# Optimization experiments

Hardware: AMD Instinct MI355X
Metric: run time of the kernel (lower is better)

## Reference

```python
import jax, jax.numpy as jnp
import numpy as np

DT = 0.02
Z_DIM = 32
U_DIM = 16


def _mlp(x, layers):
    # layers: list of (W, b); SiLU between all but last layer
    n = len(layers)
    for i, (W, b) in enumerate(layers):
        x = x @ W + b
        if i < n - 1:
            x = jax.nn.silu(x)
    return x


def _forward(x, u,
             e_w1, e_b1, e_w2, e_b2, e_w3, e_b3,
             d_w1, d_b1, d_w2, d_b2, d_w3, d_b3, d_w4, d_b4,
             a_w1, a_b1, a_w2, a_b2, a_w3, a_b3,
             b_w1, b_b1, b_w2, b_b2, b_w3, b_b3):
    # encode
    z = _mlp(x, [(e_w1, e_b1), (e_w2, e_b2), (e_w3, e_b3)])          # (B, Z)
    # state-dependent A(x) parameters: pairs (a_i, b_i) per 2x2 block
    aux = _mlp(x, [(a_w1, a_b1), (a_w2, a_b2), (a_w3, a_b3)])        # (B, Z)
    a = aux[:, 0::2]                                                  # (B, Z/2)
    b = aux[:, 1::2]
    f = jnp.exp(a * DT)
    c = jnp.cos(b * DT)
    s = jnp.sin(b * DT)
    # A(x) @ z without materializing block-diagonal: per-pair rotation-scale
    z0 = z[:, 0::2]
    z1 = z[:, 1::2]
    Az = jnp.stack([f * (c * z0 - s * z1), f * (s * z0 + c * z1)], axis=-1).reshape(z.shape)
    # B(x) @ u
    Bmat = _mlp(x, [(b_w1, b_b1), (b_w2, b_b2), (b_w3, b_b3)]).reshape(-1, Z_DIM, U_DIM)
    Bu = jnp.einsum('bzu,bu->bz', Bmat, u)
    # latent Euler step + decode
    z_next = z + DT * (Az + Bu)
    return _mlp(z_next, [(d_w1, d_b1), (d_w2, d_b2), (d_w3, d_b3), (d_w4, d_b4)])


def setup_inputs() -> dict:
    key = jax.random.key(0)
    ks = iter(jax.random.split(key, 32))
    def w(shape, scale=0.02):
        return jax.random.normal(next(ks), shape, jnp.float32) * scale
    B, X, U, Z, H, A = 16384, 64, 16, 32, 1024, 256
    return {
        'x': jax.random.normal(next(ks), (B, X), jnp.float32),
        'u': jax.random.normal(next(ks), (B, U), jnp.float32),
        'e_w1': w((X, H)), 'e_b1': w((H,)),
        'e_w2': w((H, H)), 'e_b2': w((H,)),
        'e_w3': w((H, Z)), 'e_b3': w((Z,)),
        'd_w1': w((Z, H)), 'd_b1': w((H,)),
        'd_w2': w((H, H)), 'd_b2': w((H,)),
        'd_w3': w((H, H)), 'd_b3': w((H,)),
        'd_w4': w((H, X)), 'd_b4': w((X,)),
        'a_w1': w((X, A)), 'a_b1': w((A,)),
        'a_w2': w((A, A)), 'a_b2': w((A,)),
        'a_w3': w((A, Z)), 'a_b3': w((Z,)),
        'b_w1': w((X, A)), 'b_b1': w((A,)),
        'b_w2': w((A, A)), 'b_b2': w((A,)),
        'b_w3': w((A, Z * U)), 'b_b3': w((Z * U,)),
    }


def reference(x, u,
              e_w1, e_b1, e_w2, e_b2, e_w3, e_b3,
              d_w1, d_b1, d_w2, d_b2, d_w3, d_b3, d_w4, d_b4,
              a_w1, a_b1, a_w2, a_b2, a_w3, a_b3,
              b_w1, b_b1, b_w2, b_b2, b_w3, b_b3):
    return _forward(x, u,
                    e_w1, e_b1, e_w2, e_b2, e_w3, e_b3,
                    d_w1, d_b1, d_w2, d_b2, d_w3, d_b3, d_w4, d_b4,
                    a_w1, a_b1, a_w2, a_b2, a_w3, a_b3,
                    b_w1, b_b1, b_w2, b_b2, b_w3, b_b3)
```

## Files before the change

kernel.cpp:

```cpp
#include <hip/hip_runtime.h>
#include <cstdint>
#include <cstddef>

#define B_SZ 16384
#define X_D  64
#define U_D  16
#define Z_D  32
#define H_D  1024
#define A_D  256
#define DT_C 0.02f

typedef _Float16 f16;
typedef f16   f16x8 __attribute__((ext_vector_type(8)));
typedef f16   f16x4 __attribute__((ext_vector_type(4)));
typedef float f32x4 __attribute__((ext_vector_type(4)));

#define AS1 __attribute__((address_space(1)))
#define AS3 __attribute__((address_space(3)))

__device__ __forceinline__ void gld_lds16(const void* g, void* l) {
    __builtin_amdgcn_global_load_lds((AS1 void*)(g), (AS3 void*)(l), 16, 0, 0);
}

struct GArg {
    const f16*  A;
    const f16*  W;
    const float* bias;
    void*       C;
    const float* U;
    int lda, ldc, K;
};
struct GPair { GArg g[2]; };

template<int BM,int BN,int BK,int WM,int WN,bool SILU,int OM>
__launch_bounds__(256)
__global__ void gemm_k(GPair p)
{
    static_assert(OM != 1 || BN == 128, "OM1 repack assumes BN=128");
    const GArg ga = p.g[blockIdx.z];

    constexpr int SEGROW = BK / 8;
    constexpr int SMASK  = (SEGROW < 8 ? SEGROW : 8) - 1;
    constexpr int WTM = BM / WM, WTN = BN / WN;
    constexpr int RM = WTM / 16, RN = WTN / 16;
    constexpr int ITA = (BM * SEGROW) / 256;
    constexpr int ITB = (BN * SEGROW) / 256;

    constexpr int STAGE_B = (BM + BN) * BK * 2;
    constexpr int CS_B    = (OM == 1) ? BM * BN * 2 : 0;
    constexpr int SMEM_B  = STAGE_B > CS_B ? STAGE_B : CS_B;
    __shared__ __align__(16) char smem[SMEM_B];
    f16* As = (f16*)smem;
    f16* Bs = As + BM * BK;

    const int tid  = threadIdx.x;
    const int lane = tid & 63;
    const int wave = tid >> 6;
    const int wm = wave / WN, wn = wave % WN;
    const int l15 = lane & 15, quad = lane >> 4;

    const size_t arow0 = (size_t)blockIdx.x * BM;
    const size_t brow0 = (size_t)blockIdx.y * BN;
    const int lda = ga.lda, K = ga.K;

    f32x4 zero = {0.f, 0.f, 0.f, 0.f};
    f32x4 acc[RM][RN];
#pragma unroll
    for (int i = 0; i < RM; ++i)
#pragma unroll
        for (int j = 0; j < RN; ++j) acc[i][j] = zero;

    for (int k0 = 0; k0 < K; k0 += BK) {
#pragma unroll
        for (int it = 0; it < ITA; ++it) {
            int s = it * 256 + tid;
            int row = s / SEGROW, st = s % SEGROW;
            int sg = st ^ (row & SMASK);
            gld_lds16(ga.A + (arow0 + row) * lda + k0 + sg * 8, &As[s * 8]);
        }
#pragma unroll
        for (int it = 0; it < ITB; ++it) {
            int s = it * 256 + tid;
            int row = s / SEGROW, st = s % SEGROW;
            int sg = st ^ (row & SMASK);
            gld_lds16(ga.W + (brow0 + row) * K + k0 + sg * 8, &Bs[s * 8]);
        }
        __syncthreads();

#pragma unroll
        for (int kk = 0; kk < BK; kk += 32) {
            f16x8 af[RM], bf[RN];
#pragma unroll
            for (int i = 0; i < RM; ++i) {
                int row = wm * WTM + i * 16 + l15;
                int st  = ((kk >> 3) + quad) ^ (row & SMASK);
                af[i] = *(const f16x8*)&As[(row * SEGROW + st) * 8];
            }
#pragma unroll
            for (int j = 0; j < RN; ++j) {
                int row = wn * WTN + j * 16 + l15;
                int st  = ((kk >> 3) + quad) ^ (row & SMASK);
                bf[j] = *(const f16x8*)&Bs[(row * SEGROW + st) * 8];
            }
#pragma unroll
            for (int i = 0; i < RM; ++i)
#pragma unroll
                for (int j = 0; j < RN; ++j)
                    acc[i][j] = __builtin_amdgcn_mfma_f32_16x16x32_f16(
                        af[i], bf[j], acc[i][j], 0, 0, 0);
        }
        __syncthreads();
    }

    const int rowbL = wm * WTM;
    const int colbL = wn * WTN;

    if constexpr (OM == 2) {
        const int zcol0 = ((int)brow0 + colbL) >> 4;
#pragma unroll
        for (int i = 0; i < RM; ++i) {
#pragma unroll
            for (int r = 0; r < 4; ++r) {
                int row = (int)arow0 + rowbL + i * 16 + quad * 4 + r;
                float uv = ga.U[row * 16 + l15];
#pragma unroll
                for (int j = 0; j < RN; ++j) {
                    int col = (int)brow0 + colbL + j * 16 + l15;
                    float v = (acc[i][j][r] + ga.bias[col]) * uv;
                    v += __shfl_xor(v, 8, 16);
                    v += __shfl_xor(v, 4, 16);
                    v += __shfl_xor(v, 2, 16);
                    v += __shfl_xor(v, 1, 16);
                    if (l15 == 0) ((float*)ga.C)[row * 32 + zcol0 + j] = v;
                }
            }
        }
    } else if constexpr (OM == 1) {
        f16* Cs = (f16*)smem;
#pragma unroll
        for (int j = 0; j < RN; ++j) {
            int colL = colbL + j * 16 + l15;
            float bv = ga.bias[(int)brow0 + colL];
            int chL = colL >> 3, wi = colL & 7;
#pragma unroll
            for (int i = 0; i < RM; ++i) {
#pragma unroll
                for (int r = 0; r < 4; ++r) {
                    int rowL = rowbL + i * 16 + quad * 4 + r;
                    float v = acc[i][j][r] + bv;
                    if (SILU) v = v / (1.0f + __expf(-v));
                    Cs[rowL * BN + ((chL ^ (rowL & 15)) << 3) + wi] = (f16)v;
                }
            }
        }
        __syncthreads();
        f16* Cout = (f16*)ga.C;
#pragma unroll
        for (int pass = 0; pass < (BM * BN / 8) / 256; ++pass) {
            int s = pass * 256 + tid;
            int rowL = s >> 4;
            int ch = s & 15;
            f16x8 v = *(const f16x8*)&Cs[rowL * BN + ((ch ^ (rowL & 15)) << 3)];
            *(f16x8*)&Cout[(size_t)(arow0 + rowL) * ga.ldc + brow0 + ch * 8] = v;
        }
    } else {
        float* Cout = (float*)ga.C;
#pragma unroll
        for (int j = 0; j < RN; ++j) {
            int col = (int)brow0 + colbL + j * 16 + l15;
            float bv = ga.bias[col];
#pragma unroll
            for (int i = 0; i < RM; ++i) {
#pragma unroll
                for (int r = 0; r < 4; ++r) {
                    int row = (int)arow0 + rowbL + i * 16 + quad * 4 + r;
                    float v = acc[i][j][r] + bv;
                    if (SILU) v = v / (1.0f + __expf(-v));
                    Cout[(size_t)row * ga.ldc + col] = v;
                }
            }
        }
    }
}

struct PrepArgs {
    const float* w[13];
    f16*         wt[13];
    int          K[13];
    int          N[13];
    const float* bsrc[3];
    float*       bias1;
    const float* x;
    f16*         xb;
};

__launch_bounds__(256)
__global__ void prep_k(PrepArgs pa, int ntrans, int ncvt)
{
    int bid = blockIdx.x;
    if (bid < ntrans) {
        int i = 0, t;
        for (;; ++i) {
            t = (pa.K[i] >> 5) * (pa.N[i] >> 5);
            if (bid < t) break;
            bid -= t;
        }
        const int K = pa.K[i], N = pa.N[i];
        const int tn = N >> 5;
        const int k0 = (bid / tn) << 5, n0 = (bid % tn) << 5;
        __shared__ float tbuf[32][33];
        const int tx = threadIdx.x & 31, ty = threadIdx.x >> 5;
        const float* src = pa.w[i];
        f16* dst = pa.wt[i];
#pragma unroll
        for (int r = 0; r < 32; r += 8)
            tbuf[ty + r][tx] = src[(size_t)(k0 + ty + r) * N + n0 + tx];
        __syncthreads();
#pragma unroll
        for (int r = 0; r < 32; r += 8)
            dst[(size_t)(n0 + ty + r) * K + k0 + tx] = (f16)tbuf[tx][ty + r];
    } else if (bid < ntrans + ncvt) {
        int i = ((bid - ntrans) * 256 + threadIdx.x) * 4;
        float4 v = *(const float4*)(pa.x + i);
        f16x4 o = {(f16)v.x, (f16)v.y, (f16)v.z, (f16)v.w};
        *(f16x4*)(pa.xb + i) = o;
    } else {
        int idx = (bid - ntrans - ncvt) * 256 + (int)threadIdx.x;
        float v = (idx < 1024) ? pa.bsrc[0][idx]
                : (idx < 1280) ? pa.bsrc[1][idx - 1024]
                               : pa.bsrc[2][idx - 1280];
        pa.bias1[idx] = v;
    }
}

__global__ void koopman_k(const float* __restrict__ zf, const float* __restrict__ auxf,
                          const float* __restrict__ Buf, f16* __restrict__ zn)
{
    int idx = blockIdx.x * 256 + threadIdx.x;
    int zi = idx & 31;
    int base = idx & ~1;
    float a = auxf[base], b = auxf[base + 1];
    float f = __expf(a * DT_C);
    float c = __cosf(b * DT_C);
    float s = __sinf(b * DT_C);
    float z0 = zf[base], z1 = zf[base + 1];
    float Az = (zi & 1) ? f * (s * z0 + c * z1) : f * (c * z0 - s * z1);
    zn[idx] = (f16)(zf[idx] + DT_C * (Az + Buf[idx]));
}

extern "C" void kernel_launch(void* const* d_in, const int* in_sizes, int n_in,
                              void* d_out, int out_size, void* d_ws, size_t ws_size,
                              hipStream_t stream)
{
    (void)in_sizes; (void)n_in; (void)out_size; (void)ws_size;
    const float* x    = (const float*)d_in[0];
    const float* u    = (const float*)d_in[1];
    const float* e_w1 = (const float*)d_in[2];  const float* e_b1 = (const float*)d_in[3];
    const float* e_w2 = (const float*)d_in[4];  const float* e_b2 = (const float*)d_in[5];
    const float* e_w3 = (const float*)d_in[6];  const float* e_b3 = (const float*)d_in[7];
    const float* d_w1 = (const float*)d_in[8];  const float* d_b1 = (const float*)d_in[9];
    const float* d_w2 = (const float*)d_in[10]; const float* d_b2 = (const float*)d_in[11];
    const float* d_w3 = (const float*)d_in[12]; const float* d_b3 = (const float*)d_in[13];
    const float* d_w4 = (const float*)d_in[14]; const float* d_b4 = (const float*)d_in[15];
    const float* a_w1 = (const float*)d_in[16]; const float* a_b1 = (const float*)d_in[17];
    const float* a_w2 = (const float*)d_in[18]; const float* a_b2 = (const float*)d_in[19];
    const float* a_w3 = (const float*)d_in[20]; const float* a_b3 = (const float*)d_in[21];
    const float* b_w1 = (const float*)d_in[22]; const float* b_b1 = (const float*)d_in[23];
    const float* b_w2 = (const float*)d_in[24]; const float* b_b2 = (const float*)d_in[25];
    const float* b_w3 = (const float*)d_in[26]; const float* b_b3 = (const float*)d_in[27];

    char* p = (char*)d_ws;
    auto alloc = [&](size_t nbytes) -> void* {
        void* r = (void*)p;
        p += (nbytes + 255) & ~(size_t)255;
        return r;
    };
    f16*   xb   = (f16*)  alloc((size_t)B_SZ * X_D * 2);
    f16*   cc1  = (f16*)  alloc((size_t)B_SZ * 1536 * 2);
    f16*   cc2  = (f16*)  alloc((size_t)B_SZ * 1536 * 2);
    float* zf   = (float*)alloc((size_t)B_SZ * Z_D * 4);
    float* auxf = (float*)alloc((size_t)B_SZ * Z_D * 4);
    float* Buf  = (float*)alloc((size_t)B_SZ * Z_D * 4);
    f16*   znb  = (f16*)  alloc((size_t)B_SZ * Z_D * 2);
    f16*   h1d  = cc1;
    f16*   h2d  = cc2;
    f16*   h3d  = cc1;
    f16*   W1t   = (f16*)alloc((size_t)1536 * X_D * 2);
    float* bias1 = (float*)alloc(1536 * 4);
    f16* e_w2t = (f16*)alloc((size_t)H_D * H_D * 2);
    f16* e_w3t = (f16*)alloc((size_t)Z_D * H_D * 2);
    f16* d_w1t = (f16*)alloc((size_t)H_D * Z_D * 2);
    f16* d_w2t = (f16*)alloc((size_t)H_D * H_D * 2);
    f16* d_w3t = (f16*)alloc((size_t)H_D * H_D * 2);
    f16* d_w4t = (f16*)alloc((size_t)X_D * H_D * 2);
    f16* a_w2t = (f16*)alloc((size_t)A_D * A_D * 2);
    f16* a_w3t = (f16*)alloc((size_t)Z_D * A_D * 2);
    f16* b_w2t = (f16*)alloc((size_t)A_D * A_D * 2);
    f16* b_w3t = (f16*)alloc((size_t)(Z_D * U_D) * A_D * 2);

    PrepArgs pa;
    const float* ws_[13] = {e_w1, e_w2, e_w3, d_w1, d_w2, d_w3, d_w4,
                            a_w1, a_w2, a_w3, b_w1, b_w2, b_w3};
    f16* wts_[13] = {W1t, e_w2t, e_w3t, d_w1t, d_w2t, d_w3t, d_w4t,
                     W1t + (size_t)1024 * X_D, a_w2t, a_w3t,
                     W1t + (size_t)1280 * X_D, b_w2t, b_w3t};
    int Ks_[13] = {X_D, H_D, H_D, Z_D, H_D, H_D, H_D, X_D, A_D, A_D, X_D, A_D, A_D};
    int Ns_[13] = {H_D, H_D, Z_D, H_D, H_D, H_D, X_D, A_D, A_D, Z_D, A_D, A_D, Z_D*U_D};
    int ntrans = 0;
    for (int i = 0; i < 13; ++i) {
        pa.w[i] = ws_[i]; pa.wt[i] = wts_[i]; pa.K[i] = Ks_[i]; pa.N[i] = Ns_[i];
        ntrans += (Ks_[i] >> 5) * (Ns_[i] >> 5);
    }
    pa.bsrc[0] = e_b1; pa.bsrc[1] = a_b1; pa.bsrc[2] = b_b1;
    pa.bias1 = bias1; pa.x = x; pa.xb = xb;
    const int ncvt = (B_SZ * X_D) / 1024;
    prep_k<<<ntrans + ncvt + 6, 256, 0, stream>>>(pa, ntrans, ncvt);

    auto G = [](const f16* A, const f16* W, const float* bias, void* C,
                int lda, int ldc, int K, const float* U = nullptr) {
        GArg g; g.A = A; g.W = W; g.bias = bias; g.C = C; g.U = U;
        g.lda = lda; g.ldc = ldc; g.K = K; return g;
    };
    GPair pr;

    pr.g[0] = pr.g[1] = G(xb, W1t, bias1, cc1, X_D, 1536, X_D);
    gemm_k<128,128,64,2,2,true,1><<<dim3(B_SZ/128, 1536/128, 1), 256, 0, stream>>>(pr);

    pr.g[0] = pr.g[1] = G(cc1, e_w2t, e_b2, cc2, 1536, 1536, H_D);
    gemm_k<128,128,64,2,2,true,1><<<dim3(B_SZ/128, H_D/128, 1), 256, 0, stream>>>(pr);

    pr.g[0] = G(cc1 + 1024, a_w2t, a_b2, cc2 + 1024, 1536, 1536, A_D);
    pr.g[1] = G(cc1 + 1280, b_w2t, b_b2, cc2 + 1280, 1536, 1536, A_D);
    gemm_k<128,128,64,2,2,true,1><<<dim3(B_SZ/128, A_D/128, 2), 256, 0, stream>>>(pr);

    pr.g[0] = G(cc2,        e_w3t, e_b3, zf,   1536, Z_D, H_D);
    pr.g[1] = G(cc2 + 1024, a_w3t, a_b3, auxf, 1536, Z_D, A_D);
    gemm_k<64,32,64,4,1,false,0><<<dim3(B_SZ/64, 1, 2), 256, 0, stream>>>(pr);

    pr.g[0] = pr.g[1] = G(cc2 + 1280, b_w3t, b_b3, Buf, 1536, Z_D, A_D, u);
    gemm_k<128,128,64,2,2,false,2><<<dim3(B_SZ/128, (Z_D*U_D)/128, 1), 256, 0, stream>>>(pr);

    koopman_k<<<(B_SZ * Z_D) / 256, 256, 0, stream>>>(zf, auxf, Buf, znb);

    pr.g[0] = pr.g[1] = G(znb, d_w1t, d_b1, h1d, Z_D, H_D, Z_D);
    gemm_k<128,128,32,2,2,true,1><<<dim3(B_SZ/128, H_D/128, 1), 256, 0, stream>>>(pr);

    pr.g[0] = pr.g[1] = G(h1d, d_w2t, d_b2, h2d, H_D, H_D, H_D);
    gemm_k<128,128,64,2,2,true,1><<<dim3(B_SZ/128, H_D/128, 1), 256, 0, stream>>>(pr);

    pr.g[0] = pr.g[1] = G(h2d, d_w3t, d_b3, h3d, H_D, H_D, H_D);
    gemm_k<128,128,64,2,2,true,1><<<dim3(B_SZ/128, H_D/128, 1), 256, 0, stream>>>(pr);

    pr.g[0] = pr.g[1] = G(h3d, d_w4t, d_b4, d_out, H_D, X_D, H_D);
    gemm_k<64,64,64,2,2,false,0><<<dim3(B_SZ/64, 1, 1), 256, 0, stream>>>(pr);
}
```

Before: 378.6 us.

## Use 256-row GEMM tiles and fuse Koopman step into Bu GEMM epilogue

Doubles the M tile of all main GEMMs from 128 to 256 rows. Each wave now holds twice as many accumulators, and the LDS-staged epilogue writes out in two 128-row passes to keep shared memory small. Separately, the latent Euler/rotation update is folded into the B(x)u GEMM epilogue, so the standalone koopman kernel and the Buf intermediate buffer are gone. This saves launches and global traffic and improves operand reuse, at the cost of more register pressure, possibly lower occupancy, and fewer blocks per grid.

```diff
diff --git a/kernel.cpp b/kernel.cpp
--- a/kernel.cpp
+++ b/kernel.cpp
@@ -28,6 +28,8 @@
     const float* bias;
     void*       C;
     const float* U;
+    const float* zf;
+    const float* aux;
     int lda, ldc, K;
 };
 struct GPair { GArg g[2]; };
@@ -36,7 +38,7 @@
 __launch_bounds__(256)
 __global__ void gemm_k(GPair p)
 {
-    static_assert(OM != 1 || BN == 128, "OM1 repack assumes BN=128");
+    static_assert(OM != 1 || (BM == 256 && BN == 128 && WM == 2), "OM1 shape");
     const GArg ga = p.g[blockIdx.z];
 
     constexpr int SEGROW = BK / 8;
@@ -47,7 +49,7 @@
     constexpr int ITB = (BN * SEGROW) / 256;
 
     constexpr int STAGE_B = (BM + BN) * BK * 2;
-    constexpr int CS_B    = (OM == 1) ? BM * BN * 2 : 0;
+    constexpr int CS_B    = (OM == 1) ? 128 * BN * 2 : 0;
     constexpr int SMEM_B  = STAGE_B > CS_B ? STAGE_B : CS_B;
     __shared__ __align__(16) char smem[SMEM_B];
     f16* As = (f16*)smem;
@@ -131,37 +133,55 @@
                     v += __shfl_xor(v, 4, 16);
                     v += __shfl_xor(v, 2, 16);
                     v += __shfl_xor(v, 1, 16);
-                    if (l15 == 0) ((float*)ga.C)[row * 32 + zcol0 + j] = v;
+                    if (l15 == 0) {
+                        int z = zcol0 + j;
+                        int pb = row * 32 + (z & ~1);
+                        float a  = ga.aux[pb], b = ga.aux[pb + 1];
+                        float z0 = ga.zf[pb],  z1 = ga.zf[pb + 1];
+                        float f  = __expf(a * DT_C);
+                        float c_ = __cosf(b * DT_C);
+                        float s_ = __sinf(b * DT_C);
+                        float Az = (z & 1) ? f * (s_ * z0 + c_ * z1)
+                                           : f * (c_ * z0 - s_ * z1);
+                        float zc = (z & 1) ? z1 : z0;
+                        ((f16*)ga.C)[row * 32 + z] = (f16)(zc + DT_C * (Az + v));
+                    }
                 }
             }
         }
     } else if constexpr (OM == 1) {
         f16* Cs = (f16*)smem;
-#pragma unroll
-        for (int j = 0; j < RN; ++j) {
-            int colL = colbL + j * 16 + l15;
-            float bv = ga.bias[(int)brow0 + colL];
-            int chL = colL >> 3, wi = colL & 7;
-#pragma unroll
-            for (int i = 0; i < RM; ++i) {
-#pragma unroll
-                for (int r = 0; r < 4; ++r) {
-                    int rowL = rowbL + i * 16 + quad * 4 + r;
-                    float v = acc[i][j][r] + bv;
-                    if (SILU) v = v / (1.0f + __expf(-v));
-                    Cs[rowL * BN + ((chL ^ (rowL & 15)) << 3) + wi] = (f16)v;
+        f16* Cout = (f16*)ga.C;
+#pragma unroll
+        for (int pass = 0; pass < 2; ++pass) {
+            if (wm == pass) {
+#pragma unroll
+                for (int j = 0; j < RN; ++j) {
+                    int colL = wn * WTN + j * 16 + l15;
+                    float bv = ga.bias[(int)brow0 + colL];
+                    int chL = colL >> 3, wi = colL & 7;
+#pragma unroll
+                    for (int i = 0; i < RM; ++i) {
+#pragma unroll
+                        for (int r = 0; r < 4; ++r) {
+                            int rowL = i * 16 + quad * 4 + r;
+                            float v = acc[i][j][r] + bv;
+                            if (SILU) v = v / (1.0f + __expf(-v));
+                            Cs[rowL * BN + ((chL ^ (rowL & 15)) << 3) + wi] = (f16)v;
+                        }
+                    }
                 }
             }
-        }
-        __syncthreads();
-        f16* Cout = (f16*)ga.C;
-#pragma unroll
-        for (int pass = 0; pass < (BM * BN / 8) / 256; ++pass) {
-            int s = pass * 256 + tid;
-            int rowL = s >> 4;
-            int ch = s & 15;
-            f16x8 v = *(const f16x8*)&Cs[rowL * BN + ((ch ^ (rowL & 15)) << 3)];
-            *(f16x8*)&Cout[(size_t)(arow0 + rowL) * ga.ldc + brow0 + ch * 8] = v;
+            __syncthreads();
+#pragma unroll
+            for (int it = 0; it < (128 * BN / 8) / 256; ++it) {
+                int s = it * 256 + tid;
+                int rowL = s >> 4, ch = s & 15;
+                f16x8 v = *(const f16x8*)&Cs[rowL * BN + ((ch ^ (rowL & 15)) << 3)];
+                *(f16x8*)&Cout[(size_t)(arow0 + pass * 128 + rowL) * ga.ldc
+                               + brow0 + ch * 8] = v;
+            }
+            __syncthreads();
         }
     } else {
         float* Cout = (float*)ga.C;
@@ -231,21 +251,6 @@
                                : pa.bsrc[2][idx - 1280];
         pa.bias1[idx] = v;
     }
-}
-
-__global__ void koopman_k(const float* __restrict__ zf, const float* __restrict__ auxf,
-                          const float* __restrict__ Buf, f16* __restrict__ zn)
-{
-    int idx = blockIdx.x * 256 + threadIdx.x;
-    int zi = idx & 31;
-    int base = idx & ~1;
-    float a = auxf[base], b = auxf[base + 1];
-    float f = __expf(a * DT_C);
-    float c = __cosf(b * DT_C);
-    float s = __sinf(b * DT_C);
-    float z0 = zf[base], z1 = zf[base + 1];
-    float Az = (zi & 1) ? f * (s * z0 + c * z1) : f * (c * z0 - s * z1);
-    zn[idx] = (f16)(zf[idx] + DT_C * (Az + Buf[idx]));
 }
 
 extern "C" void kernel_launch(void* const* d_in, const int* in_sizes, int n_in,
@@ -280,7 +285,6 @@
     f16*   cc2  = (f16*)  alloc((size_t)B_SZ * 1536 * 2);
     float* zf   = (float*)alloc((size_t)B_SZ * Z_D * 4);
     float* auxf = (float*)alloc((size_t)B_SZ * Z_D * 4);
-    float* Buf  = (float*)alloc((size_t)B_SZ * Z_D * 4);
     f16*   znb  = (f16*)  alloc((size_t)B_SZ * Z_D * 2);
     f16*   h1d  = cc1;
     f16*   h2d  = cc2;
@@ -317,39 +321,38 @@
     prep_k<<<ntrans + ncvt + 6, 256, 0, stream>>>(pa, ntrans, ncvt);
 
     auto G = [](const f16* A, const f16* W, const float* bias, void* C,
-                int lda, int ldc, int K, const float* U = nullptr) {
+                int lda, int ldc, int K, const float* U = nullptr,
+                const float* zf_ = nullptr, const float* aux_ = nullptr) {
         GArg g; g.A = A; g.W = W; g.bias = bias; g.C = C; g.U = U;
-        g.lda = lda; g.ldc = ldc; g.K = K; return g;
+        g.zf = zf_; g.aux = aux_; g.lda = lda; g.ldc = ldc; g.K = K; return g;
     };
     GPair pr;
 
     pr.g[0] = pr.g[1] = G(xb, W1t, bias1, cc1, X_D, 1536, X_D);
-    gemm_k<128,128,64,2,2,true,1><<<dim3(B_SZ/128, 1536/128, 1), 256, 0, stream>>>(pr);
+    gemm_k<256,128,64,2,2,true,1><<<dim3(B_SZ/256, 1536/128, 1), 256, 0, stream>>>(pr);
 
     pr.g[0] = pr.g[1] = G(cc1, e_w2t, e_b2, cc2, 1536, 1536, H_D);
-    gemm_k<128,128,64,2,2,true,1><<<dim3(B_SZ/128, H_D/128, 1), 256, 0, stream>>>(pr);
+    gemm_k<256,128,64,2,2,true,1><<<dim3(B_SZ/256, H_D/128, 1), 256, 0, stream>>>(pr);
 
     pr.g[0] = G(cc1 + 1024, a_w2t, a_b2, cc2 + 1024, 1536, 1536, A_D);
     pr.g[1] = G(cc1 + 1280, b_w2t, b_b2, cc2 + 1280, 1536, 1536, A_D);
-    gemm_k<128,128,64,2,2,true,1><<<dim3(B_SZ/128, A_D/128, 2), 256, 0, stream>>>(pr);
+    gemm_k<256,128,64,2,2,true,1><<<dim3(B_SZ/256, A_D/128, 2), 256, 0, stream>>>(pr);
 
     pr.g[0] = G(cc2,        e_w3t, e_b3, zf,   1536, Z_D, H_D);
     pr.g[1] = G(cc2 + 1024, a_w3t, a_b3, auxf, 1536, Z_D, A_D);
     gemm_k<64,32,64,4,1,false,0><<<dim3(B_SZ/64, 1, 2), 256, 0, stream>>>(pr);
 
-    pr.g[0] = pr.g[1] = G(cc2 + 1280, b_w3t, b_b3, Buf, 1536, Z_D, A_D, u);
-    gemm_k<128,128,64,2,2,false,2><<<dim3(B_SZ/128, (Z_D*U_D)/128, 1), 256, 0, stream>>>(pr);
-
-    koopman_k<<<(B_SZ * Z_D) / 256, 256, 0, stream>>>(zf, auxf, Buf, znb);
+    pr.g[0] = pr.g[1] = G(cc2 + 1280, b_w3t, b_b3, znb, 1536, Z_D, A_D, u, zf, auxf);
+    gemm_k<256,128,64,2,2,false,2><<<dim3(B_SZ/256, (Z_D*U_D)/128, 1), 256, 0, stream>>>(pr);
 
     pr.g[0] = pr.g[1] = G(znb, d_w1t, d_b1, h1d, Z_D, H_D, Z_D);
-    gemm_k<128,128,32,2,2,true,1><<<dim3(B_SZ/128, H_D/128, 1), 256, 0, stream>>>(pr);
+    gemm_k<256,128,32,2,2,true,1><<<dim3(B_SZ/256, H_D/128, 1), 256, 0, stream>>>(pr);
 
     pr.g[0] = pr.g[1] = G(h1d, d_w2t, d_b2, h2d, H_D, H_D, H_D);
-    gemm_k<128,128,64,2,2,true,1><<<dim3(B_SZ/128, H_D/128, 1), 256, 0, stream>>>(pr);
+    gemm_k<256,128,64,2,2,true,1><<<dim3(B_SZ/256, H_D/128, 1), 256, 0, stream>>>(pr);
 
     pr.g[0] = pr.g[1] = G(h2d, d_w3t, d_b3, h3d, H_D, H_D, H_D);
-    gemm_k<128,128,64,2,2,true,1><<<dim3(B_SZ/128, H_D/128, 1), 256, 0, stream>>>(pr);
+    gemm_k<256,128,64,2,2,true,1><<<dim3(B_SZ/256, H_D/128, 1), 256, 0, stream>>>(pr);
 
     pr.g[0] = pr.g[1] = G(h3d, d_w4t, d_b4, d_out, H_D, X_D, H_D);
     gemm_k<64,64,64,2,2,false,0><<<dim3(B_SZ/64, 1, 1), 256, 0, stream>>>(pr);
```

New measurement: 674.4 us. 1.78x slower.

## Fuse latent heads and Koopman step into one kernel; merge layer-2 GEMMs

Applied to the files above, without the earlier changes.

Replaces the encoder output GEMM, aux output GEMM, B(x)u GEMM and the Koopman elementwise kernel with a single mid_k kernel that works on 32-row tiles and keeps z, aux and Bu in shared memory before writing the f16 latent. It also merges the three second-layer GEMMs (encoder, aux, B-net) into one launch using a y-index split across three argument sets. This cuts kernel launches and the fp32 intermediate round-trips through global memory. The cost is a small-tile fused kernel with lower MFMA efficiency, in which the B-head weights are reloaded per 32-row block.

```diff
diff --git a/kernel.cpp b/kernel.cpp
--- a/kernel.cpp
+++ b/kernel.cpp
@@ -27,17 +27,18 @@
     const f16*  W;
     const float* bias;
     void*       C;
-    const float* U;
     int lda, ldc, K;
 };
-struct GPair { GArg g[2]; };
+struct GSet { GArg g[3]; int yn0, yn1; };
 
 template<int BM,int BN,int BK,int WM,int WN,bool SILU,int OM>
 __launch_bounds__(256)
-__global__ void gemm_k(GPair p)
+__global__ void gemm_k(GSet p)
 {
     static_assert(OM != 1 || BN == 128, "OM1 repack assumes BN=128");
-    const GArg ga = p.g[blockIdx.z];
+    int yb = blockIdx.y, gi = 0;
+    if (yb >= p.yn0) { yb -= p.yn0; gi = 1; if (yb >= p.yn1) { yb -= p.yn1; gi = 2; } }
+    const GArg ga = p.g[gi];
 
     constexpr int SEGROW = BK / 8;
     constexpr int SMASK  = (SEGROW < 8 ? SEGROW : 8) - 1;
@@ -60,7 +61,7 @@
     const int l15 = lane & 15, quad = lane >> 4;
 
     const size_t arow0 = (size_t)blockIdx.x * BM;
-    const size_t brow0 = (size_t)blockIdx.y * BN;
+    const size_t brow0 = (size_t)yb * BN;
     const int lda = ga.lda, K = ga.K;
 
     f32x4 zero = {0.f, 0.f, 0.f, 0.f};
@@ -115,27 +116,7 @@
     const int rowbL = wm * WTM;
     const int colbL = wn * WTN;
 
-    if constexpr (OM == 2) {
-        const int zcol0 = ((int)brow0 + colbL) >> 4;
-#pragma unroll
-        for (int i = 0; i < RM; ++i) {
-#pragma unroll
-            for (int r = 0; r < 4; ++r) {
-                int row = (int)arow0 + rowbL + i * 16 + quad * 4 + r;
-                float uv = ga.U[row * 16 + l15];
-#pragma unroll
-                for (int j = 0; j < RN; ++j) {
-                    int col = (int)brow0 + colbL + j * 16 + l15;
-                    float v = (acc[i][j][r] + ga.bias[col]) * uv;
-                    v += __shfl_xor(v, 8, 16);
-                    v += __shfl_xor(v, 4, 16);
-                    v += __shfl_xor(v, 2, 16);
-                    v += __shfl_xor(v, 1, 16);
-                    if (l15 == 0) ((float*)ga.C)[row * 32 + zcol0 + j] = v;
-                }
-            }
-        }
-    } else if constexpr (OM == 1) {
+    if constexpr (OM == 1) {
         f16* Cs = (f16*)smem;
 #pragma unroll
         for (int j = 0; j < RN; ++j) {
@@ -180,6 +161,149 @@
                 }
             }
         }
+    }
+}
+
+__launch_bounds__(256)
+__global__ void mid_k(const f16* __restrict__ cc2,
+                      const f16* __restrict__ e_w3t, const float* __restrict__ e_b3,
+                      const f16* __restrict__ a_w3t, const float* __restrict__ a_b3,
+                      const f16* __restrict__ b_w3t, const float* __restrict__ b_b3,
+                      const float* __restrict__ u,   f16* __restrict__ znb)
+{
+    __shared__ __align__(16) f16 As[32 * 64];
+    __shared__ __align__(16) f16 Bs[128 * 64];
+    __shared__ float zb[32 * 32];
+    __shared__ float ab[32 * 32];
+    __shared__ float bu[32 * 32];
+    __shared__ float ub[32 * 16];
+
+    const int tid  = threadIdx.x;
+    const int lane = tid & 63, wave = tid >> 6;
+    const int l15 = lane & 15, quad = lane >> 4;
+    const int r0 = blockIdx.x * 32;
+
+    ub[tid]       = u[r0 * 16 + tid];
+    ub[tid + 256] = u[r0 * 16 + 256 + tid];
+
+#pragma unroll 1
+    for (int ph = 0; ph < 2; ++ph) {
+        const f16* W    = ph ? a_w3t : e_w3t;
+        const float* bs = ph ? a_b3 : e_b3;
+        const int K     = ph ? 256 : 1024;
+        const int co    = ph ? 1024 : 0;
+        float* ob       = ph ? ab : zb;
+        f32x4 acc = {0.f, 0.f, 0.f, 0.f};
+        for (int k0 = 0; k0 < K; k0 += 64) {
+            {
+                int row = tid >> 3, sg = (tid & 7) ^ (row & 7);
+                gld_lds16(cc2 + (size_t)(r0 + row) * 1536 + co + k0 + sg * 8,
+                          &As[tid * 8]);
+            }
+            {
+                int row = tid >> 3, sg = (tid & 7) ^ (row & 7);
+                gld_lds16(W + (size_t)row * K + k0 + sg * 8, &Bs[tid * 8]);
+            }
+            __syncthreads();
+#pragma unroll
+            for (int kk = 0; kk < 64; kk += 32) {
+                int ar = ((wave >> 1) << 4) + l15;
+                int ast = ((kk >> 3) + quad) ^ (ar & 7);
+                f16x8 af = *(const f16x8*)&As[(ar * 8 + ast) * 8];
+                int br = ((wave & 1) << 4) + l15;
+                int bst = ((kk >> 3) + quad) ^ (br & 7);
+                f16x8 bf = *(const f16x8*)&Bs[(br * 8 + bst) * 8];
+                acc = __builtin_amdgcn_mfma_f32_16x16x32_f16(af, bf, acc, 0, 0, 0);
+            }
+            __syncthreads();
+        }
+#pragma unroll
+        for (int r = 0; r < 4; ++r) {
+            int row = ((wave >> 1) << 4) + quad * 4 + r;
+            int col = ((wave & 1) << 4) + l15;
+            ob[row * 32 + col] = acc[r] + bs[col];
+        }
+    }
+
+#pragma unroll 1
+    for (int ch = 0; ch < 4; ++ch) {
+        f32x4 acc[2][2];
+#pragma unroll
+        for (int i = 0; i < 2; ++i)
+#pragma unroll
+            for (int j = 0; j < 2; ++j) acc[i][j] = f32x4{0.f, 0.f, 0.f, 0.f};
+        for (int k0 = 0; k0 < 256; k0 += 64) {
+            {   int row = tid >> 3, sg = (tid & 7) ^ (row & 7);
+                gld_lds16(cc2 + (size_t)(r0 + row) * 1536 + 1280 + k0 + sg * 8,
+                          &As[tid * 8]);
+            }
+#pragma unroll
+            for (int it = 0; it < 4; ++it) {
+                int s = it * 256 + tid;
+                int row = s >> 3, sg = (s & 7) ^ (row & 7);
+                gld_lds16(b_w3t + (size_t)(ch * 128 + row) * 256 + k0 + sg * 8,
+                          &Bs[s * 8]);
+            }
+            __syncthreads();
+#pragma unroll
+            for (int kk = 0; kk < 64; kk += 32) {
+                f16x8 af[2], bf[2];
+#pragma unroll
+                for (int i = 0; i < 2; ++i) {
+                    int ar = i * 16 + l15;
+                    int st = ((kk >> 3) + quad) ^ (ar & 7);
+                    af[i] = *(const f16x8*)&As[(ar * 8 + st) * 8];
+                }
+#pragma unroll
+                for (int j = 0; j < 2; ++j) {
+                    int br = wave * 32 + j * 16 + l15;
+                    int st = ((kk >> 3) + quad) ^ (br & 7);
+                    bf[j] = *(const f16x8*)&Bs[(br * 8 + st) * 8];
+                }
+#pragma unroll
+                for (int i = 0; i < 2; ++i)
+#pragma unroll
+                    for (int j = 0; j < 2; ++j)
+                        acc[i][j] = __builtin_amdgcn_mfma_f32_16x16x32_f16(
+                            af[i], bf[j], acc[i][j], 0, 0, 0);
+            }
+            __syncthreads();
+        }
+#pragma unroll
+        for (int j = 0; j < 2; ++j) {
+            int colg = ch * 128 + wave * 32 + j * 16 + l15;
+            float bv = b_b3[colg];
+            int z = colg >> 4;
+#pragma unroll
+            for (int i = 0; i < 2; ++i) {
+#pragma unroll
+                for (int r = 0; r < 4; ++r) {
+                    int row = i * 16 + quad * 4 + r;
+                    float v = (acc[i][j][r] + bv) * ub[row * 16 + l15];
+                    v += __shfl_xor(v, 8, 16);
+                    v += __shfl_xor(v, 4, 16);
+                    v += __shfl_xor(v, 2, 16);
+                    v += __shfl_xor(v, 1, 16);
+                    if (l15 == 0) bu[row * 32 + z] = v;
+                }
+            }
+        }
+    }
+    __syncthreads();
+
+#pragma unroll
+    for (int t = 0; t < 4; ++t) {
+        int idx = t * 256 + tid;
+        int row = idx >> 5, z = idx & 31;
+        int pb = idx & ~1;
+        float a  = ab[pb], b = ab[pb + 1];
+        float z0 = zb[pb], z1 = zb[pb + 1];
+        float f  = __expf(a * DT_C);
+        float c_ = __cosf(b * DT_C);
+        float s_ = __sinf(b * DT_C);
+        float Az = (z & 1) ? f * (s_ * z0 + c_ * z1) : f * (c_ * z0 - s_ * z1);
+        float zc = (z & 1) ? z1 : z0;
+        znb[(size_t)(r0 + row) * 32 + z] = (f16)(zc + DT_C * (Az + bu[idx]));
     }
 }
 
@@ -231,21 +355,6 @@
                                : pa.bsrc[2][idx - 1280];
         pa.bias1[idx] = v;
     }
-}
-
-__global__ void koopman_k(const float* __restrict__ zf, const float* __restrict__ auxf,
-                          const float* __restrict__ Buf, f16* __restrict__ zn)
-{
-    int idx = blockIdx.x * 256 + threadIdx.x;
-    int zi = idx & 31;
-    int base = idx & ~1;
-    float a = auxf[base], b = auxf[base + 1];
-    float f = __expf(a * DT_C);
-    float c = __cosf(b * DT_C);
-    float s = __sinf(b * DT_C);
-    float z0 = zf[base], z1 = zf[base + 1];
-    float Az = (zi & 1) ? f * (s * z0 + c * z1) : f * (c * z0 - s * z1);
-    zn[idx] = (f16)(zf[idx] + DT_C * (Az + Buf[idx]));
 }
 
 extern "C" void kernel_launch(void* const* d_in, const int* in_sizes, int n_in,
@@ -278,9 +387,6 @@
     f16*   xb   = (f16*)  alloc((size_t)B_SZ * X_D * 2);
     f16*   cc1  = (f16*)  alloc((size_t)B_SZ * 1536 * 2);
     f16*   cc2  = (f16*)  alloc((size_t)B_SZ * 1536 * 2);
-    float* zf   = (float*)alloc((size_t)B_SZ * Z_D * 4);
-    float* auxf = (float*)alloc((size_t)B_SZ * Z_D * 4);
-    float* Buf  = (float*)alloc((size_t)B_SZ * Z_D * 4);
     f16*   znb  = (f16*)  alloc((size_t)B_SZ * Z_D * 2);
     f16*   h1d  = cc1;
     f16*   h2d  = cc2;
@@ -317,40 +423,36 @@
     prep_k<<<ntrans + ncvt + 6, 256, 0, stream>>>(pa, ntrans, ncvt);
 
     auto G = [](const f16* A, const f16* W, const float* bias, void* C,
-                int lda, int ldc, int K, const float* U = nullptr) {
-        GArg g; g.A = A; g.W = W; g.bias = bias; g.C = C; g.U = U;
+                int lda, int ldc, int K) {
+        GArg g; g.A = A; g.W = W; g.bias = bias; g.C = C;
         g.lda = lda; g.ldc = ldc; g.K = K; return g;
     };
-    GPair pr;
-
-    pr.g[0] = pr.g[1] = G(xb, W1t, bias1, cc1, X_D, 1536, X_D);
-    gemm_k<128,128,64,2,2,true,1><<<dim3(B_SZ/128, 1536/128, 1), 256, 0, stream>>>(pr);
-
-    pr.g[0] = pr.g[1] = G(cc1, e_w2t, e_b2, cc2, 1536, 1536, H_D);
-    gemm_k<128,128,64,2,2,true,1><<<dim3(B_SZ/128, H_D/128, 1), 256, 0, stream>>>(pr);
-
-    pr.g[0] = G(cc1 + 1024, a_w2t, a_b2, cc2 + 1024, 1536, 1536, A_D);
-    pr.g[1] = G(cc1 + 1280, b_w2t, b_b2, cc2 + 1280, 1536, 1536, A_D);
-    gemm_k<128,128,64,2,2,true,1><<<dim3(B_SZ/128, A_D/128, 2), 256, 0, stream>>>(pr);
-
-    pr.g[0] = G(cc2,        e_w3t, e_b3, zf,   1536, Z_D, H_D);
-    pr.g[1] = G(cc2 + 1024, a_w3t, a_b3, auxf, 1536, Z_D, A_D);
-    gemm_k<64,32,64,4,1,false,0><<<dim3(B_SZ/64, 1, 2), 256, 0, stream>>>(pr);
-
-    pr.g[0] = pr.g[1] = G(cc2 + 1280, b_w3t, b_b3, Buf, 1536, Z_D, A_D, u);
-    gemm_k<128,128,64,2,2,false,2><<<dim3(B_SZ/128, (Z_D*U_D)/128, 1), 256, 0, stream>>>(pr);
-
-    koopman_k<<<(B_SZ * Z_D) / 256, 256, 0, stream>>>(zf, auxf, Buf, znb);
-
-    pr.g[0] = pr.g[1] = G(znb, d_w1t, d_b1, h1d, Z_D, H_D, Z_D);
-    gemm_k<128,128,32,2,2,true,1><<<dim3(B_SZ/128, H_D/128, 1), 256, 0, stream>>>(pr);
-
-    pr.g[0] = pr.g[1] = G(h1d, d_w2t, d_b2, h2d, H_D, H_D, H_D);
-    gemm_k<128,128,64,2,2,true,1><<<dim3(B_SZ/128, H_D/128, 1), 256, 0, stream>>>(pr);
-
-    pr.g[0] = pr.g[1] = G(h2d, d_w3t, d_b3, h3d, H_D, H_D, H_D);
-    gemm_k<128,128,64,2,2,true,1><<<dim3(B_SZ/128, H_D/128, 1), 256, 0, stream>>>(pr);
-
-    pr.g[0] = pr.g[1] = G(h3d, d_w4t, d_b4, d_out, H_D, X_D, H_D);
-    gemm_k<64,64,64,2,2,false,0><<<dim3(B_SZ/64, 1, 1), 256, 0, stream>>>(pr);
+    GSet s;
+
+    s.g[0] = G(xb, W1t, bias1, cc1, X_D, 1536, X_D);
+    s.yn0 = 12; s.yn1 = 0;
+    gemm_k<128,128,64,2,2,true,1><<<dim3(B_SZ/128, 12), 256, 0, stream>>>(s);
+
+    s.g[0] = G(cc1,        e_w2t, e_b2, cc2,        1536, 1536, H_D);
+    s.g[1] = G(cc1 + 1024, a_w2t, a_b2, cc2 + 1024, 1536, 1536, A_D);
+    s.g[2] = G(cc1 + 1280, b_w2t, b_b2, cc2 + 1280, 1536, 1536, A_D);
+    s.yn0 = 8; s.yn1 = 2;
+    gemm_k<128,128,64,2,2,true,1><<<dim3(B_SZ/128, 12), 256, 0, stream>>>(s);
+
+    mid_k<<<B_SZ/32, 256, 0, stream>>>(cc2, e_w3t, e_b3, a_w3t, a_b3,
+                                       b_w3t, b_b3, u, znb);
+
+    s.yn0 = 8; s.yn1 = 0;
+    s.g[0] = G(znb, d_w1t, d_b1, h1d, Z_D, H_D, Z_D);
+    gemm_k<128,128,32,2,2,true,1><<<dim3(B_SZ/128, 8), 256, 0, stream>>>(s);
+
+    s.g[0] = G(h1d, d_w2t, d_b2, h2d, H_D, H_D, H_D);
+    gemm_k<128,128,64,2,2,true,1><<<dim3(B_SZ/128, 8), 256, 0, stream>>>(s);
+
+    s.g[0] = G(h2d, d_w3t, d_b3, h3d, H_D, H_D, H_D);
+    gemm_k<128,128,64,2,2,true,1><<<dim3(B_SZ/128, 8), 256, 0, stream>>>(s);
+
+    s.g[0] = G(h3d, d_w4t, d_b4, d_out, H_D, X_D, H_D);
+    s.yn0 = 1;
+    gemm_k<64,64,64,2,2,false,0><<<dim3(B_SZ/64, 1), 256, 0, stream>>>(s);
 }
```

After: 370.9 us. -2.1%, faster.
